# Kernel tuning notes

Measured on AMD Instinct MI355X. Metric: run time of the kernel, lower is better.

## Reference

```python
import jax, jax.numpy as jnp
import numpy as np

B, Q, K, H, V = 32, 64, 512, 64, 64
NEG = -1e6


def setup_inputs() -> dict:
    key = jax.random.key(0)
    ks = jax.random.split(key, 7)
    queries = jax.random.normal(ks[0], (B, Q, H), dtype=jnp.float32)
    keys = jax.random.normal(ks[1], (B, K, H), dtype=jnp.float32)
    values = jax.random.normal(ks[2], (B, K, V), dtype=jnp.float32)
    valid_lens = jax.random.randint(ks[3], (B,), 1, K + 1, dtype=jnp.int32)
    # Linear weights stored as (in_features, out_features); x @ W == torch Linear
    Wq = jax.random.normal(ks[4], (H, H), dtype=jnp.float32) / np.sqrt(H)
    Wk = jax.random.normal(ks[5], (H, H), dtype=jnp.float32) / np.sqrt(H)
    wv = jax.random.normal(ks[6], (H,), dtype=jnp.float32) / np.sqrt(H)
    return {"queries": queries, "keys": keys, "values": values,
            "valid_lens": valid_lens, "Wq": Wq, "Wk": Wk, "wv": wv}


def reference(queries, keys, values, valid_lens, Wq, Wk, wv):
    q = jnp.einsum('bqd,dh->bqh', queries, Wq)          # (B,Q,H)
    k = jnp.einsum('bkd,dh->bkh', keys, Wk)             # (B,K,H)
    # additive (Bahdanau) features: (B,Q,K,H) broadcast intermediate
    feats = jnp.tanh(q[:, :, None, :] + k[:, None, :, :])
    scores = jnp.einsum('bqkh,h->bqk', feats, wv)       # (B,Q,K)
    # masked softmax over key axis: positions >= valid_len get -1e6
    mask = jnp.arange(K)[None, :] < valid_lens[:, None]  # (B,K)
    scores = jnp.where(mask[:, None, :], scores, NEG)
    attn = jax.nn.softmax(scores, axis=-1)              # (B,Q,K)
    return jnp.einsum('bqk,bkv->bqv', attn, values)     # (B,Q,V)
```

## Files before the change

kernel.cpp:

```cpp
#include <hip/hip_runtime.h>
#include <hip/hip_bf16.h>

#define NEG (-1e6f)

static constexpr int B = 32, Q = 64, K = 512, H = 64, V = 64;
static constexpr float C2LE = 2.8853900817779268f;
static constexpr float L2E  = 1.4426950408889634f;

typedef __attribute__((ext_vector_type(8))) short bf16x8;
typedef __attribute__((ext_vector_type(4))) float f32x4;

__device__ __forceinline__ float fexp2(float x) { return __builtin_amdgcn_exp2f(x); }
__device__ __forceinline__ float frcp(float x)  { return __builtin_amdgcn_rcpf(x); }

__device__ __forceinline__ unsigned pk(float a, float b) {
  __hip_bfloat162 h = __float22bfloat162_rn(make_float2(a, b));
  return *reinterpret_cast<unsigned*>(&h);
}
union bfrag { unsigned u[4]; bf16x8 v; };

__global__ __launch_bounds__(256) void proj_kernel(
    const float* __restrict__ queries, const float* __restrict__ keys,
    const float* __restrict__ Wq, const float* __restrict__ Wk,
    const float* __restrict__ wv, const int* __restrict__ vlens,
    float* __restrict__ qAR2, unsigned* __restrict__ Ekp)
{
  __shared__ float Wl[64 * 65];
  const int xcd = blockIdx.x & 7, slot = blockIdx.x >> 3;
  const bool isQ = slot < 4;
  const int idx = slot - 4;
  const int b = isQ ? (xcd * 4 + slot) : (xcd * 4 + (idx & 3));
  const int kb64 = idx >> 2;
  const int vlen = vlens[b];
  if (!isQ && kb64 * 64 >= vlen) return;

  const int tid = threadIdx.x, lane = tid & 63;
  const int wave = __builtin_amdgcn_readfirstlane(tid >> 6);
  const float* Wsrc = isQ ? Wq : Wk;
  #pragma unroll
  for (int i = 0; i < 16; ++i) {
    const int j = tid + i * 256;
    Wl[(j >> 6) * 65 + (j & 63)] = Wsrc[j];
  }
  __syncthreads();

  const int r = lane & 15, g = lane >> 4;
  const int rloc0 = (isQ ? 0 : kb64 * 64) + wave * 16;
  if (!isQ && rloc0 >= vlen) return;
  const float* xbase = isQ ? (queries + ((size_t)b * Q + rloc0) * H)
                           : (keys    + ((size_t)b * K + rloc0) * H);

  bf16x8 afr[2];
  #pragma unroll
  for (int kb = 0; kb < 2; ++kb) {
    const float* px = xbase + (size_t)r * H + kb * 32 + g * 8;
    const float4 x0 = *(const float4*)px;
    const float4 x1 = *(const float4*)(px + 4);
    bfrag a;
    a.u[0] = pk(x0.x, x0.y); a.u[1] = pk(x0.z, x0.w);
    a.u[2] = pk(x1.x, x1.y); a.u[3] = pk(x1.z, x1.w);
    afr[kb] = a.v;
  }

  #pragma unroll
  for (int t = 0; t < 4; ++t) {
    const int hcol = t * 16 + r;
    f32x4 acc = {0.f, 0.f, 0.f, 0.f};
    #pragma unroll
    for (int kb = 0; kb < 2; ++kb) {
      const float* wp = &Wl[(kb * 32 + g * 8) * 65 + hcol];
      bfrag w;
      #pragma unroll
      for (int jj = 0; jj < 4; ++jj)
        w.u[jj] = pk(wp[(2*jj) * 65], wp[(2*jj + 1) * 65]);
      acc = isQ ? __builtin_amdgcn_mfma_f32_16x16x32_bf16(afr[kb], w.v, acc, 0, 0, 0)
                : __builtin_amdgcn_mfma_f32_16x16x32_bf16(w.v, afr[kb], acc, 0, 0, 0);
    }
    if (isQ) {
      const float wvv = wv[hcol];
      #pragma unroll
      for (int rr = 0; rr < 4; ++rr) {
        const int qq = rloc0 + g * 4 + rr;
        const float s = fminf(15.f, fmaxf(-15.f, acc[rr])) * C2LE;
        const float rq = fexp2(-s);
        const size_t off = (((size_t)(b * 16 + (qq >> 2)) * 32 + (hcol >> 1)) * 16)
                           + (qq & 3) * 4 + (hcol & 1) * 2;
        *(float2*)(qAR2 + off) = make_float2(-2.f * wvv * rq, rq);
      }
    } else {
      const int k = rloc0 + r;
      float E[4];
      #pragma unroll
      for (int rr = 0; rr < 4; ++rr)
        E[rr] = fexp2(fminf(15.f, fmaxf(-15.f, acc[rr])) * C2LE);
      const int hp = t * 8 + g * 2;
      Ekp[((size_t)b * 32 + hp    ) * 512 + k] = pk(E[0], E[1]);
      Ekp[((size_t)b * 32 + hp + 1) * 512 + k] = pk(E[2], E[3]);
    }
  }
}

__global__ __launch_bounds__(512) void attn_kernel(
    const float* __restrict__ qAR2, const unsigned* __restrict__ Ekp,
    const float* __restrict__ values, const int* __restrict__ vlens,
    float* __restrict__ out)
{
  __shared__ unsigned ekl[32 * 512];
  __shared__ float red[4][2][2];

  const int xcd = blockIdx.x & 7, slot = blockIdx.x >> 3;
  const int b  = xcd * 4 + ((slot + (slot >> 5)) & 3);
  const int qg = slot >> 2;
  const int vlen = vlens[b];
  const int tid = threadIdx.x, lane = tid & 63;
  const int wave = __builtin_amdgcn_readfirstlane(tid >> 6);

  {
    const unsigned* src = Ekp + (size_t)b * 32 * 512;
    #pragma unroll
    for (int i = 0; i < 8; ++i) {
      const int c = i * 8 + wave;
      if ((c & 1) * 256 < vlen) {
        const uint4 v = *(const uint4*)(src + c * 256 + lane * 4);
        *(uint4*)&ekl[c * 256 + lane * 4] = v;
      }
    }
  }
  __syncthreads();

  float a0 = 0.f, a1 = 0.f, a2 = 0.f, a3 = 0.f;
  if (wave * 64 < vlen) {
    const float* ar = qAR2 +
        (size_t)__builtin_amdgcn_readfirstlane((b * 16 + qg) * 512);
    #pragma unroll
    for (int hp = 0; hp < 32; ++hp) {
      const unsigned u = ekl[hp * 512 + tid];
      const float E0 = __uint_as_float(u << 16);
      const float E1 = __uint_as_float(u & 0xffff0000u);
      const float* s = ar + hp * 16;
      a0 = fmaf(s[ 0], frcp(s[ 1] + E0), a0);
      a0 = fmaf(s[ 2], frcp(s[ 3] + E1), a0);
      a1 = fmaf(s[ 4], frcp(s[ 5] + E0), a1);
      a1 = fmaf(s[ 6], frcp(s[ 7] + E1), a1);
      a2 = fmaf(s[ 8], frcp(s[ 9] + E0), a2);
      a2 = fmaf(s[10], frcp(s[11] + E1), a2);
      a3 = fmaf(s[12], frcp(s[13] + E0), a3);
      a3 = fmaf(s[14], frcp(s[15] + E1), a3);
    }
  }
  __syncthreads();
  float* p    = (float*)ekl;
  float* part = (float*)ekl + 2048;
  if (wave * 64 < vlen) {
    p[0 * 512 + tid] = a0; p[1 * 512 + tid] = a1;
    p[2 * 512 + tid] = a2; p[3 * 512 + tid] = a3;
  }
  __syncthreads();

  const int qi = wave & 3, half = wave >> 2;
  const int kb2 = half * 256 + lane * 4;
  {
    float s[4];
    *(float4*)s = *(const float4*)&p[qi * 512 + kb2];
    float m = NEG;
    #pragma unroll
    for (int j = 0; j < 4; ++j) {
      s[j] = (kb2 + j < vlen) ? s[j] : NEG;
      m = fmaxf(m, s[j]);
    }
    #pragma unroll
    for (int off = 32; off; off >>= 1) m = fmaxf(m, __shfl_xor(m, off, 64));
    if (lane == 0) red[qi][half][0] = m;
    __syncthreads();
    m = fmaxf(red[qi][0][0], red[qi][1][0]);
    float sum = 0.f;
    #pragma unroll
    for (int j = 0; j < 4; ++j) { s[j] = fexp2((s[j] - m) * L2E); sum += s[j]; }
    *(float4*)&p[qi * 512 + kb2] = *(float4*)s;
    #pragma unroll
    for (int off = 32; off; off >>= 1) sum += __shfl_xor(sum, off, 64);
    if (lane == 0) red[qi][half][1] = sum;
    __syncthreads();
  }

  {
    const int chunk = ((vlen + 31) >> 5) << 2;
    const int kb = wave * chunk;
    const float* vb = values + ((size_t)b * K + kb) * V + lane;
    float c0 = 0.f, c1 = 0.f, c2 = 0.f, c3 = 0.f;
    #pragma unroll 4
    for (int k4 = 0; k4 < chunk; k4 += 4) {
      const float4 p0 = *(const float4*)&p[0 * 512 + kb + k4];
      const float4 p1 = *(const float4*)&p[1 * 512 + kb + k4];
      const float4 p2 = *(const float4*)&p[2 * 512 + kb + k4];
      const float4 p3 = *(const float4*)&p[3 * 512 + kb + k4];
      const float v0 = vb[(size_t)(k4 + 0) * V];
      const float v1 = vb[(size_t)(k4 + 1) * V];
      const float v2 = vb[(size_t)(k4 + 2) * V];
      const float v3 = vb[(size_t)(k4 + 3) * V];
      c0 = fmaf(p0.x,v0, fmaf(p0.y,v1, fmaf(p0.z,v2, fmaf(p0.w,v3, c0))));
      c1 = fmaf(p1.x,v0, fmaf(p1.y,v1, fmaf(p1.z,v2, fmaf(p1.w,v3, c1))));
      c2 = fmaf(p2.x,v0, fmaf(p2.y,v1, fmaf(p2.z,v2, fmaf(p2.w,v3, c2))));
      c3 = fmaf(p3.x,v0, fmaf(p3.y,v1, fmaf(p3.z,v2, fmaf(p3.w,v3, c3))));
    }
    part[(wave*4+0)*64+lane] = c0; part[(wave*4+1)*64+lane] = c1;
    part[(wave*4+2)*64+lane] = c2; part[(wave*4+3)*64+lane] = c3;
  }
  __syncthreads();

  if (wave < 4) {
    const float inv = frcp(red[wave][0][1] + red[wave][1][1]);
    float o = 0.f;
    #pragma unroll
    for (int w = 0; w < 8; ++w) o += part[(w*4+wave)*64 + lane];
    out[((size_t)b * Q + qg * 4 + wave) * V + lane] = o * inv;
  }
}

extern "C" void kernel_launch(void* const* d_in, const int* in_sizes, int n_in,
                              void* d_out, int out_size, void* d_ws, size_t ws_size,
                              hipStream_t stream) {
  const float* queries = (const float*)d_in[0];
  const float* keys    = (const float*)d_in[1];
  const float* values  = (const float*)d_in[2];
  const int*   vlens   = (const int*)d_in[3];
  const float* Wq      = (const float*)d_in[4];
  const float* Wk      = (const float*)d_in[5];
  const float* wv      = (const float*)d_in[6];
  float* out = (float*)d_out;

  float*    qAR2 = (float*)d_ws;
  unsigned* Ekp  = (unsigned*)(qAR2 + (size_t)B*16*512);

  proj_kernel<<<288, 256, 0, stream>>>(queries, keys, Wq, Wk, wv, vlens, qAR2, Ekp);
  attn_kernel<<<512, 512, 0, stream>>>(qAR2, Ekp, values, vlens, out);
}
```

Before: 23.61 us.

## Split projection into single-wave blocks reading weights directly from global

The projection kernel now launches 1152 single-wave blocks, each handling one 16-row strip, instead of 288 four-wave blocks. The shared-memory staging of the weight matrix and its block barrier are removed, and each lane reads its weight fragments straight from global memory (L2/L1 cached). This aims to raise parallelism, skip more fully masked key strips at finer granularity, and drop the barrier and LDS copy. The cost is strided uncoalesced global reads of W repeated by every block.

```diff
diff --git a/kernel.cpp b/kernel.cpp
--- a/kernel.cpp
+++ b/kernel.cpp
@@ -19,36 +19,23 @@
 }
 union bfrag { unsigned u[4]; bf16x8 v; };
 
-__global__ __launch_bounds__(256) void proj_kernel(
+__global__ __launch_bounds__(64) void proj_kernel(
     const float* __restrict__ queries, const float* __restrict__ keys,
     const float* __restrict__ Wq, const float* __restrict__ Wk,
     const float* __restrict__ wv, const int* __restrict__ vlens,
     float* __restrict__ qAR2, unsigned* __restrict__ Ekp)
 {
-  __shared__ float Wl[64 * 65];
-  const int xcd = blockIdx.x & 7, slot = blockIdx.x >> 3;
-  const bool isQ = slot < 4;
-  const int idx = slot - 4;
-  const int b = isQ ? (xcd * 4 + slot) : (xcd * 4 + (idx & 3));
-  const int kb64 = idx >> 2;
-  const int vlen = vlens[b];
-  if (!isQ && kb64 * 64 >= vlen) return;
-
-  const int tid = threadIdx.x, lane = tid & 63;
-  const int wave = __builtin_amdgcn_readfirstlane(tid >> 6);
-  const float* Wsrc = isQ ? Wq : Wk;
-  #pragma unroll
-  for (int i = 0; i < 16; ++i) {
-    const int j = tid + i * 256;
-    Wl[(j >> 6) * 65 + (j & 63)] = Wsrc[j];
-  }
-  __syncthreads();
-
+  const int xcd = blockIdx.x & 7, u = blockIdx.x >> 3;
+  const bool isQ = u < 16;
+  const int b   = xcd * 4 + (isQ ? (u >> 2) : ((u - 16) & 3));
+  const int str = isQ ? (u & 3) : ((u - 16) >> 2);
+  if (!isQ && str * 16 >= vlens[b]) return;
+
+  const int lane = threadIdx.x & 63;
   const int r = lane & 15, g = lane >> 4;
-  const int rloc0 = (isQ ? 0 : kb64 * 64) + wave * 16;
-  if (!isQ && rloc0 >= vlen) return;
-  const float* xbase = isQ ? (queries + ((size_t)b * Q + rloc0) * H)
-                           : (keys    + ((size_t)b * K + rloc0) * H);
+  const float* W = isQ ? Wq : Wk;
+  const float* xbase = isQ ? (queries + ((size_t)b * Q + str * 16) * H)
+                           : (keys    + ((size_t)b * K + str * 16) * H);
 
   bf16x8 afr[2];
   #pragma unroll
@@ -68,11 +55,11 @@
     f32x4 acc = {0.f, 0.f, 0.f, 0.f};
     #pragma unroll
     for (int kb = 0; kb < 2; ++kb) {
-      const float* wp = &Wl[(kb * 32 + g * 8) * 65 + hcol];
       bfrag w;
       #pragma unroll
       for (int jj = 0; jj < 4; ++jj)
-        w.u[jj] = pk(wp[(2*jj) * 65], wp[(2*jj + 1) * 65]);
+        w.u[jj] = pk(W[(kb * 32 + g * 8 + 2*jj    ) * H + hcol],
+                     W[(kb * 32 + g * 8 + 2*jj + 1) * H + hcol]);
       acc = isQ ? __builtin_amdgcn_mfma_f32_16x16x32_bf16(afr[kb], w.v, acc, 0, 0, 0)
                 : __builtin_amdgcn_mfma_f32_16x16x32_bf16(w.v, afr[kb], acc, 0, 0, 0);
     }
@@ -80,7 +67,7 @@
       const float wvv = wv[hcol];
       #pragma unroll
       for (int rr = 0; rr < 4; ++rr) {
-        const int qq = rloc0 + g * 4 + rr;
+        const int qq = str * 16 + g * 4 + rr;
         const float s = fminf(15.f, fmaxf(-15.f, acc[rr])) * C2LE;
         const float rq = fexp2(-s);
         const size_t off = (((size_t)(b * 16 + (qq >> 2)) * 32 + (hcol >> 1)) * 16)
@@ -88,7 +75,7 @@
         *(float2*)(qAR2 + off) = make_float2(-2.f * wvv * rq, rq);
       }
     } else {
-      const int k = rloc0 + r;
+      const int k = str * 16 + r;
       float E[4];
       #pragma unroll
       for (int rr = 0; rr < 4; ++rr)
@@ -232,6 +219,6 @@
   float*    qAR2 = (float*)d_ws;
   unsigned* Ekp  = (unsigned*)(qAR2 + (size_t)B*16*512);
 
-  proj_kernel<<<288, 256, 0, stream>>>(queries, keys, Wq, Wk, wv, vlens, qAR2, Ekp);
+  proj_kernel<<<1152, 64, 0, stream>>>(queries, keys, Wq, Wk, wv, vlens, qAR2, Ekp);
   attn_kernel<<<512, 512, 0, stream>>>(qAR2, Ekp, values, vlens, out);
 }
```

Measured after the change: 23.59 us. No clear change (-0.1%).
